# Kernel tuning notes

Hardware: AMD Instinct MI355X
Metric: run time of the kernel (lower is better)

## Reference

```python
import math
import jax, jax.numpy as jnp
import numpy as np

B, T, D = 2, 2048, 2048
H = 16
HD = D // H  # 128


def setup_inputs() -> dict:
    key = jax.random.key(0)
    k1, k2, k3 = jax.random.split(key, 3)
    x = jax.random.normal(k1, (B, T, D), dtype=jnp.float32)
    # Linear weights stored as [in, out] for x @ W (torch Linear weight is [out,in])
    w_attn = jax.random.normal(k2, (D, 3 * D), dtype=jnp.float32) * (1.0 / math.sqrt(D))
    w_proj = jax.random.normal(k3, (D, D), dtype=jnp.float32) * (1.0 / math.sqrt(D))
    return {"x": x, "w_attn": w_attn, "w_proj": w_proj}


def reference(x, w_attn, w_proj):
    Bc, Tc, Dc = x.shape
    qkv = x @ w_attn  # [B, T, 3D]
    q, k, v = jnp.split(qkv, 3, axis=2)
    # [B, H, T, HD]
    q = q.reshape(Bc, Tc, H, HD).transpose(0, 2, 1, 3)
    k = k.reshape(Bc, Tc, H, HD).transpose(0, 2, 1, 3)
    v = v.reshape(Bc, Tc, H, HD).transpose(0, 2, 1, 3)
    att = jnp.einsum('bhqd,bhkd->bhqk', q, k) * (1.0 / math.sqrt(HD))
    causal = jnp.tril(jnp.ones((Tc, Tc), dtype=bool))
    att = jnp.where(causal[None, None], att, -jnp.inf)
    att = jax.nn.softmax(att, axis=-1)
    y = jnp.einsum('bhqk,bhkd->bhqd', att, v)
    y = y.transpose(0, 2, 1, 3).reshape(Bc, Tc, Dc)
    return y @ w_proj
```

## Files before the change

kernel.cpp:

```cpp
#include <hip/hip_runtime.h>
#include <hip/hip_bf16.h>

#define B_ 2
#define T_ 2048
#define D_ 2048
#define H_ 16
#define HD_ 128
#define N3_ (3 * D_)
#define M_ (B_ * T_)

typedef __attribute__((ext_vector_type(8))) short short8;
typedef __attribute__((ext_vector_type(4))) short short4v;
typedef __attribute__((ext_vector_type(4))) float floatx4;

__device__ __forceinline__ ushort f2bf(float f) {
  unsigned int x = __float_as_uint(f);
  unsigned int r = (x + 0x7fffu + ((x >> 16) & 1u)) >> 16;
  return (ushort)r;
}

__device__ __forceinline__ void gload_lds16(const ushort* g, ushort* l) {
  __builtin_amdgcn_global_load_lds(
      (const __attribute__((address_space(1))) void*)g,
      (__attribute__((address_space(3))) void*)l, 16, 0, 0);
}

#define CONVB 4096
#define WATB 12288
#define WPTB 4096
__global__ __launch_bounds__(256) void prep(const float* __restrict__ x,
                                            const float* __restrict__ wa,
                                            const float* __restrict__ wp,
                                            ushort* __restrict__ xb,
                                            ushort* __restrict__ wt_attn,
                                            ushort* __restrict__ wt_proj) {
  __shared__ ushort tile[32][33];
  int bid = blockIdx.x;
  if (bid < CONVB) {
    int i = bid * 2048 + threadIdx.x * 8;
    union { ushort u[8]; short8 v; } t;
#pragma unroll
    for (int j = 0; j < 8; j++) t.u[j] = f2bf(x[i + j]);
    *(short8*)(xb + i) = t.v;
    return;
  }
  const float* in;
  ushort* out;
  int N, bx, by;
  if (bid < CONVB + WATB) {
    int id = bid - CONVB;
    N = N3_; bx = id % 192; by = id / 192; in = wa; out = wt_attn;
  } else {
    int id = bid - (CONVB + WATB);
    N = D_; bx = id & 63; by = id >> 6; in = wp; out = wt_proj;
  }
  int n0 = bx * 32, k0 = by * 32;
  int tx = threadIdx.x & 31, ty = threadIdx.x >> 5;
#pragma unroll
  for (int i = ty; i < 32; i += 8)
    tile[i][tx] = f2bf(in[(size_t)(k0 + i) * N + n0 + tx]);
  __syncthreads();
#pragma unroll
  for (int i = ty; i < 32; i += 8)
    out[(size_t)(n0 + i) * 2048 + k0 + tx] = tile[tx][i];
}

#define GBM 256
#define GBN 128
#define GBK 64
#define GKD 2048
#define GNT (GKD / GBK)
#define A_US (GBM * GBK)
#define B_US (GBN * GBK)
#define BUF_US (A_US + B_US)

struct GPtr {
  const ushort* a0;
  const ushort* b0;
};

__device__ __forceinline__ void gstage(const GPtr& gp, size_t kpos,
                                       ushort* slot, int w512) {
#pragma unroll
  for (int j = 0; j < 4; j++)
    gload_lds16(gp.a0 + kpos + (size_t)j * 64 * GKD, slot + j * 4096 + w512);
#pragma unroll
  for (int j = 0; j < 2; j++)
    gload_lds16(gp.b0 + kpos + (size_t)j * 64 * GKD,
                slot + A_US + j * 4096 + w512);
}

template <int VM, bool STG, bool BAR>
__device__ __forceinline__ void kstep(const GPtr& gp, size_t kpos,
                                      const ushort* Ac, const ushort* Bc,
                                      ushort* sslot, int w512,
                                      const int (&aoff)[4][2],
                                      const int (&boff)[4][2],
                                      floatx4 (&acc)[4][4]) {
  short8 af[4][2], bf[4][2];
#pragma unroll
  for (int kk = 0; kk < 2; kk++)
#pragma unroll
    for (int i = 0; i < 4; i++) {
      af[i][kk] = *(const short8*)(Ac + aoff[i][kk]);
      bf[i][kk] = *(const short8*)(Bc + boff[i][kk]);
    }
  if constexpr (STG) gstage(gp, kpos, sslot, w512);
  __builtin_amdgcn_s_setprio(1);
#pragma unroll
  for (int kk = 0; kk < 2; kk++)
#pragma unroll
    for (int mi = 0; mi < 4; mi++)
#pragma unroll
      for (int nj = 0; nj < 4; nj++)
        acc[mi][nj] = __builtin_amdgcn_mfma_f32_16x16x32_bf16(
            af[mi][kk], bf[nj][kk], acc[mi][nj], 0, 0, 0);
  __builtin_amdgcn_s_setprio(0);
  if constexpr (VM == 6) {
    asm volatile("s_waitcnt vmcnt(6)" ::: "memory");
  } else if constexpr (VM == 0) {
    asm volatile("s_waitcnt vmcnt(0)" ::: "memory");
  }
  if constexpr (BAR) {
    __builtin_amdgcn_sched_barrier(0);
    __builtin_amdgcn_s_barrier();
    __builtin_amdgcn_sched_barrier(0);
  }
}

__device__ __forceinline__ void gemm_core(const ushort* __restrict__ Ag,
                                          const ushort* __restrict__ Bg,
                                          ushort* lds, floatx4 (&acc)[4][4]) {
  int tid = threadIdx.x;
  int lane = tid & 63, wave = tid >> 6;
  int l16 = lane & 15, quad = lane >> 4;
  int wr = wave >> 1, wc = wave & 1;
  int w512 = wave * 512;

  int swz = ((tid & 7) ^ ((tid >> 3) & 7)) * 8;
  GPtr gp;
  gp.a0 = Ag + (size_t)(tid >> 3) * GKD + swz;
  gp.b0 = Bg + (size_t)(tid >> 3) * GKD + swz;

  int aoff[4][2], boff[4][2];
#pragma unroll
  for (int i = 0; i < 4; i++)
#pragma unroll
    for (int kk = 0; kk < 2; kk++) {
      int chk = ((kk * 4 + quad) ^ (l16 & 7)) * 8;
      aoff[i][kk] = (wr * 64 + i * 16 + l16) * GBK + chk;
      boff[i][kk] = (wc * 64 + i * 16 + l16) * GBK + chk;
    }

  gstage(gp, 0, lds, w512);
  gstage(gp, GBK, lds + BUF_US, w512);
  asm volatile("s_waitcnt vmcnt(6)" ::: "memory");
  __builtin_amdgcn_sched_barrier(0);
  __builtin_amdgcn_s_barrier();
  __builtin_amdgcn_sched_barrier(0);

  const ushort* cp = lds;
  ushort* sp = lds + 2 * BUF_US;
#pragma unroll 1
  for (int t = 0; t < GNT - 2; ++t) {
    kstep<6, true, true>(gp, (size_t)(t + 2) * GBK, cp, cp + A_US, sp, w512,
                         aoff, boff, acc);
    cp = (cp == lds + 2 * BUF_US) ? lds : cp + BUF_US;
    sp = (sp == lds + 2 * BUF_US) ? lds : sp + BUF_US;
  }
  kstep<0, false, true>(gp, 0, cp, cp + A_US, lds, w512, aoff, boff, acc);
  cp = (cp == lds + 2 * BUF_US) ? lds : cp + BUF_US;
  kstep<-1, false, false>(gp, 0, cp, cp + A_US, lds, w512, aoff, boff, acc);
}

__global__ __launch_bounds__(512, 2) void gemm_qkv(const ushort* __restrict__ X,
                                                   const ushort* __restrict__ Wt,
                                                   ushort* __restrict__ qb,
                                                   ushort* __restrict__ kb,
                                                   ushort* __restrict__ vst) {
  __shared__ __align__(16) ushort lds[3 * BUF_US];
  floatx4 acc[4][4];
#pragma unroll
  for (int i = 0; i < 4; i++)
#pragma unroll
    for (int j = 0; j < 4; j++) acc[i][j] = (floatx4){0.f, 0.f, 0.f, 0.f};

  int m0 = blockIdx.y * GBM, n0 = blockIdx.x * GBN;
  gemm_core(X + (size_t)m0 * GKD, Wt + (size_t)n0 * GKD, lds, acc);

  int tid = threadIdx.x, lane = tid & 63, wave = tid >> 6;
  int l16 = lane & 15, quad = lane >> 4, wr = wave >> 1, wc = wave & 1;
  int region = n0 >> 11;
  int h = (n0 & 2047) >> 7;
  int b = m0 >> 11, tb = m0 & 2047;
  if (region == 0) {
    ushort* P = qb + ((size_t)(b * H_ + h) * T_ + tb) * HD_;
#pragma unroll
    for (int mi = 0; mi < 4; mi++)
#pragma unroll
      for (int nj = 0; nj < 4; nj++)
#pragma unroll
        for (int r = 0; r < 4; r++)
          P[(size_t)(wr * 64 + mi * 16 + quad * 4 + r) * HD_ + wc * 64 +
            nj * 16 + l16] = f2bf(acc[mi][nj][r]);
  } else if (region == 1) {
    ushort* base = kb + (size_t)(b * H_ + h) * T_ * HD_;
#pragma unroll
    for (int mi = 0; mi < 4; mi++)
#pragma unroll
      for (int nj = 0; nj < 4; nj++) {
        int d = wc * 64 + nj * 16 + l16;
        int dhi = d >> 5, dlo = d & 31;
#pragma unroll
        for (int r = 0; r < 4; r++) {
          int t = tb + wr * 64 + mi * 16 + quad * 4 + r;
          int sK = ((quad * 4 + r) >> 1) & 3;
          base[(size_t)(t >> 6) * 8192 + dhi * 2048 + (t & 63) * 32 +
               (dlo ^ (sK << 3))] = f2bf(acc[mi][nj][r]);
        }
      }
  } else {
    ushort* base = vst + (size_t)(b * H_ + h) * T_ * HD_;
    int sd = ((l16 >> 1) & 3) << 3;
#pragma unroll
    for (int mi = 0; mi < 4; mi++)
#pragma unroll
      for (int r = 0; r < 4; r++) {
        int t = tb + wr * 64 + mi * 16 + quad * 4 + r;
        int c = t & 63;
        int p = (c & 15) * 4 + (c >> 4);
        size_t rowbase =
            (size_t)(t >> 6) * 8192 + (p >> 5) * 4096 + ((p & 31) ^ sd);
#pragma unroll
        for (int nj = 0; nj < 4; nj++) {
          int d = wc * 64 + nj * 16 + l16;
          base[rowbase + d * 32] = f2bf(acc[mi][nj][r]);
        }
      }
  }
}

__global__ __launch_bounds__(512, 2) void gemm_proj(const ushort* __restrict__ Y,
                                                    const ushort* __restrict__ Wt,
                                                    float* __restrict__ out) {
  __shared__ __align__(16) ushort lds[3 * BUF_US];
  floatx4 acc[4][4];
#pragma unroll
  for (int i = 0; i < 4; i++)
#pragma unroll
    for (int j = 0; j < 4; j++) acc[i][j] = (floatx4){0.f, 0.f, 0.f, 0.f};

  int m0 = blockIdx.y * GBM, n0 = blockIdx.x * GBN;
  gemm_core(Y + (size_t)m0 * GKD, Wt + (size_t)n0 * GKD, lds, acc);

  int tid = threadIdx.x, lane = tid & 63, wave = tid >> 6;
  int l16 = lane & 15, quad = lane >> 4, wr = wave >> 1, wc = wave & 1;
#pragma unroll
  for (int mi = 0; mi < 4; mi++)
#pragma unroll
    for (int nj = 0; nj < 4; nj++)
#pragma unroll
      for (int r = 0; r < 4; r++)
        out[(size_t)(m0 + wr * 64 + mi * 16 + quad * 4 + r) * D_ + n0 +
            wc * 64 + nj * 16 + l16] = acc[mi][nj][r];
}

__global__ __launch_bounds__(256) void attn128(const ushort* __restrict__ qb,
                                               const ushort* __restrict__ kst,
                                               const ushort* __restrict__ vst,
                                               ushort* __restrict__ y) {
  __shared__ ushort Ks[2][8192];
  __shared__ ushort Vs[2][8192];
  __shared__ ushort Ps[8192];
  int bid = blockIdx.x;
  int bh = bid & 31;
  int qt = (bid < 256) ? (bid >> 5) : (15 - ((bid - 256) >> 5));
  int q0 = qt * 128;
  int tid = threadIdx.x, lane = tid & 63, wave = tid >> 6;
  int l16 = lane & 15, quad = lane >> 4;
  int b = bh >> 4, h = bh & 15;
  const ushort* Q = qb + (size_t)bh * T_ * HD_;
  const ushort* Kt = kst + (size_t)bh * T_ * HD_;
  const ushort* Vt = vst + (size_t)bh * T_ * HD_;
  int qw0 = q0 + wave * 32;

  short8 qf[2][4];
#pragma unroll
  for (int mi = 0; mi < 2; mi++)
#pragma unroll
    for (int kk = 0; kk < 4; kk++)
      qf[mi][kk] = *(const short8*)(Q + (size_t)(qw0 + mi * 16 + l16) * HD_ +
                                    kk * 32 + quad * 8);

  floatx4 o[2][8];
#pragma unroll
  for (int mi = 0; mi < 2; mi++)
#pragma unroll
    for (int nt = 0; nt < 8; nt++) o[mi][nt] = (floatx4){0.f, 0.f, 0.f, 0.f};
  float lrow[2][4];
#pragma unroll
  for (int mi = 0; mi < 2; mi++)
#pragma unroll
    for (int r = 0; r < 4; r++) lrow[mi][r] = 0.f;

  const float scale2 = 0.08838834764831845f * 1.4426950408889634f;
  int ktiles = (q0 >> 6) + 2;
  int vchk = (quad ^ ((l16 >> 1) & 3)) * 8;

#pragma unroll
  for (int i = 0; i < 4; i++) {
    int g = i * 256 + wave * 64;
    gload_lds16(Kt + (g + lane) * 8, Ks[0] + g * 8);
    gload_lds16(Vt + (g + lane) * 8, Vs[0] + g * 8);
  }
  __syncthreads();

  int cur = 0;
  for (int tile = 0; tile < ktiles; tile++) {
    int kt = tile << 6;
    if (tile + 1 < ktiles) {
#pragma unroll
      for (int i = 0; i < 4; i++) {
        int g = i * 256 + wave * 64;
        gload_lds16(Kt + (size_t)(tile + 1) * 8192 + (g + lane) * 8,
                    Ks[cur ^ 1] + g * 8);
        gload_lds16(Vt + (size_t)(tile + 1) * 8192 + (g + lane) * 8,
                    Vs[cur ^ 1] + g * 8);
      }
    }
    if (kt <= qw0 + 31) {
      const ushort* Ksb = Ks[cur];
      const ushort* Vsb = Vs[cur];
      floatx4 s[2][4];
#pragma unroll
      for (int mi = 0; mi < 2; mi++)
#pragma unroll
        for (int ng = 0; ng < 4; ng++) s[mi][ng] = (floatx4){0.f, 0.f, 0.f, 0.f};
#pragma unroll
      for (int kk = 0; kk < 4; kk++) {
        short8 kf[4];
#pragma unroll
        for (int ng = 0; ng < 4; ng++)
          kf[ng] = *(const short8*)(Ksb + kk * 2048 + (ng * 16 + l16) * 32 +
                                    vchk);
        __builtin_amdgcn_s_setprio(1);
#pragma unroll
        for (int mi = 0; mi < 2; mi++)
#pragma unroll
          for (int ng = 0; ng < 4; ng++)
            s[mi][ng] = __builtin_amdgcn_mfma_f32_16x16x32_bf16(
                qf[mi][kk], kf[ng], s[mi][ng], 0, 0, 0);
        __builtin_amdgcn_s_setprio(0);
      }
      if (kt + 63 > qw0) {
#pragma unroll
        for (int mi = 0; mi < 2; mi++)
#pragma unroll
          for (int ng = 0; ng < 4; ng++)
#pragma unroll
            for (int r = 0; r < 4; r++) {
              int key = kt + ng * 16 + l16;
              int qr = qw0 + mi * 16 + quad * 4 + r;
              float p =
                  (key <= qr) ? exp2f(s[mi][ng][r] * scale2) : 0.f;
              s[mi][ng][r] = p;
              lrow[mi][r] += p;
            }
      } else {
#pragma unroll
        for (int mi = 0; mi < 2; mi++)
#pragma unroll
          for (int ng = 0; ng < 4; ng++)
#pragma unroll
            for (int r = 0; r < 4; r++) {
              float p = exp2f(s[mi][ng][r] * scale2);
              s[mi][ng][r] = p;
              lrow[mi][r] += p;
            }
      }
      ushort* Pw = Ps + wave * 2048;
#pragma unroll
      for (int mi = 0; mi < 2; mi++)
#pragma unroll
        for (int r = 0; r < 4; r++) {
          int row = mi * 16 + quad * 4 + r;
          short4v pk;
#pragma unroll
          for (int ng = 0; ng < 4; ng++) pk[ng] = (short)f2bf(s[mi][ng][r]);
          *(short4v*)(Pw + row * 64 + (((l16 >> 1) ^ (row & 7)) << 3) +
                      ((l16 & 1) << 2)) = pk;
        }
      short8 pf[2][2];
#pragma unroll
      for (int mi = 0; mi < 2; mi++)
#pragma unroll
        for (int kc = 0; kc < 2; kc++) {
          int row = mi * 16 + l16;
          pf[mi][kc] = *(const short8*)(
              Pw + row * 64 + ((((kc << 2) + quad) ^ (row & 7)) << 3));
        }
#pragma unroll
      for (int kc = 0; kc < 2; kc++) {
#pragma unroll
        for (int nt = 0; nt < 8; nt++) {
          short8 vf = *(const short8*)(Vsb + kc * 4096 + (nt * 16 + l16) * 32 +
                                       vchk);
          __builtin_amdgcn_s_setprio(1);
#pragma unroll
          for (int mi = 0; mi < 2; mi++)
            o[mi][nt] = __builtin_amdgcn_mfma_f32_16x16x32_bf16(
                pf[mi][kc], vf, o[mi][nt], 0, 0, 0);
          __builtin_amdgcn_s_setprio(0);
        }
      }
    }
    __syncthreads();
    cur ^= 1;
  }

#pragma unroll
  for (int off = 1; off < 16; off <<= 1)
#pragma unroll
    for (int mi = 0; mi < 2; mi++)
#pragma unroll
      for (int r = 0; r < 4; r++)
        lrow[mi][r] += __shfl_xor(lrow[mi][r], off);

#pragma unroll
  for (int mi = 0; mi < 2; mi++)
#pragma unroll
    for (int r = 0; r < 4; r++) {
      float inv = 1.f / lrow[mi][r];
      int t = qw0 + mi * 16 + quad * 4 + r;
#pragma unroll
      for (int nt = 0; nt < 8; nt++)
        y[((size_t)(b * T_ + t)) * D_ + h * HD_ + nt * 16 + l16] =
            f2bf(o[mi][nt][r] * inv);
    }
}

extern "C" void kernel_launch(void* const* d_in, const int* in_sizes, int n_in,
                              void* d_out, int out_size, void* d_ws,
                              size_t ws_size, hipStream_t stream) {
  const float* x = (const float*)d_in[0];
  const float* w_attn = (const float*)d_in[1];
  const float* w_proj = (const float*)d_in[2];
  float* out = (float*)d_out;

  char* ws = (char*)d_ws;
  ushort* wt_attn = (ushort*)(ws);
  ushort* wt_proj = (ushort*)(ws + 25165824);
  ushort* qb = (ushort*)(ws + 33554432);
  ushort* kb = (ushort*)(ws + 50331648);
  ushort* vst = (ushort*)(ws + 67108864);
  ushort* xb = (ushort*)(ws + 83886080);
  ushort* yb = xb;
  (void)in_sizes; (void)n_in; (void)out_size; (void)ws_size;

  prep<<<CONVB + WATB + WPTB, 256, 0, stream>>>(x, w_attn, w_proj, xb,
                                                wt_attn, wt_proj);
  gemm_qkv<<<dim3(N3_ / GBN, M_ / GBM), 512, 0, stream>>>(xb, wt_attn, qb, kb,
                                                          vst);
  attn128<<<B_ * H_ * (T_ / 128), 256, 0, stream>>>(qb, kb, vst, yb);
  gemm_proj<<<dim3(D_ / GBN, M_ / GBM), 512, 0, stream>>>(yb, wt_proj, out);
}
```

Before: 371.1 us.

## Read K/V tiles directly from global memory in attention, dropping LDS staging

The attention kernel no longer stages K and V tiles into double-buffered shared memory with a block-wide barrier per tile. Each wave now reads its K and V fragments straight from global memory and loops only over the key tiles its own rows need, so per-tile __syncthreads disappears and LDS use shrinks. The cost is that the four waves of a block each issue redundant global/L2 reads for the same K/V data, and there is no prefetch to hide that load latency. The GEMM macros are renamed with no functional change.

```diff
diff --git a/kernel.cpp b/kernel.cpp
--- a/kernel.cpp
+++ b/kernel.cpp
@@ -8,6 +8,7 @@
 #define HD_ 128
 #define N3_ (3 * D_)
 #define M_ (B_ * T_)
+#define GKD 2048
 
 typedef __attribute__((ext_vector_type(8))) short short8;
 typedef __attribute__((ext_vector_type(4))) short short4v;
@@ -65,21 +66,17 @@
     out[(size_t)(n0 + i) * 2048 + k0 + tx] = tile[tx][i];
 }
 
-#define GBM 256
-#define GBN 128
-#define GBK 64
-#define GKD 2048
-#define GNT (GKD / GBK)
-#define A_US (GBM * GBK)
-#define B_US (GBN * GBK)
-#define BUF_US (A_US + B_US)
-
-struct GPtr {
-  const ushort* a0;
-  const ushort* b0;
-};
-
-__device__ __forceinline__ void gstage(const GPtr& gp, size_t kpos,
+#define PBM 256
+#define PBN 128
+#define PBK 64
+#define PNT (GKD / PBK)
+#define PA_US (PBM * PBK)
+#define PB_US (PBN * PBK)
+#define PBUF (PA_US + PB_US)
+
+struct PPtr { const ushort *a0, *b0; };
+
+__device__ __forceinline__ void pstage(const PPtr& gp, size_t kpos,
                                        ushort* slot, int w512) {
 #pragma unroll
   for (int j = 0; j < 4; j++)
@@ -87,11 +84,11 @@
 #pragma unroll
   for (int j = 0; j < 2; j++)
     gload_lds16(gp.b0 + kpos + (size_t)j * 64 * GKD,
-                slot + A_US + j * 4096 + w512);
+                slot + PA_US + j * 4096 + w512);
 }
 
 template <int VM, bool STG, bool BAR>
-__device__ __forceinline__ void kstep(const GPtr& gp, size_t kpos,
+__device__ __forceinline__ void pstep(const PPtr& gp, size_t kpos,
                                       const ushort* Ac, const ushort* Bc,
                                       ushort* sslot, int w512,
                                       const int (&aoff)[4][2],
@@ -105,7 +102,7 @@
       af[i][kk] = *(const short8*)(Ac + aoff[i][kk]);
       bf[i][kk] = *(const short8*)(Bc + boff[i][kk]);
     }
-  if constexpr (STG) gstage(gp, kpos, sslot, w512);
+  if constexpr (STG) pstage(gp, kpos, sslot, w512);
   __builtin_amdgcn_s_setprio(1);
 #pragma unroll
   for (int kk = 0; kk < 2; kk++)
@@ -128,9 +125,9 @@
   }
 }
 
-__device__ __forceinline__ void gemm_core(const ushort* __restrict__ Ag,
-                                          const ushort* __restrict__ Bg,
-                                          ushort* lds, floatx4 (&acc)[4][4]) {
+__device__ __forceinline__ void pgemm_core(const ushort* __restrict__ Ag,
+                                           const ushort* __restrict__ Bg,
+                                           ushort* lds, floatx4 (&acc)[4][4]) {
   int tid = threadIdx.x;
   int lane = tid & 63, wave = tid >> 6;
   int l16 = lane & 15, quad = lane >> 4;
@@ -138,7 +135,7 @@
   int w512 = wave * 512;
 
   int swz = ((tid & 7) ^ ((tid >> 3) & 7)) * 8;
-  GPtr gp;
+  PPtr gp;
   gp.a0 = Ag + (size_t)(tid >> 3) * GKD + swz;
   gp.b0 = Bg + (size_t)(tid >> 3) * GKD + swz;
 
@@ -148,29 +145,29 @@
 #pragma unroll
     for (int kk = 0; kk < 2; kk++) {
       int chk = ((kk * 4 + quad) ^ (l16 & 7)) * 8;
-      aoff[i][kk] = (wr * 64 + i * 16 + l16) * GBK + chk;
-      boff[i][kk] = (wc * 64 + i * 16 + l16) * GBK + chk;
-    }
-
-  gstage(gp, 0, lds, w512);
-  gstage(gp, GBK, lds + BUF_US, w512);
+      aoff[i][kk] = (wr * 64 + i * 16 + l16) * PBK + chk;
+      boff[i][kk] = (wc * 64 + i * 16 + l16) * PBK + chk;
+    }
+
+  pstage(gp, 0, lds, w512);
+  pstage(gp, PBK, lds + PBUF, w512);
   asm volatile("s_waitcnt vmcnt(6)" ::: "memory");
   __builtin_amdgcn_sched_barrier(0);
   __builtin_amdgcn_s_barrier();
   __builtin_amdgcn_sched_barrier(0);
 
   const ushort* cp = lds;
-  ushort* sp = lds + 2 * BUF_US;
+  ushort* sp = lds + 2 * PBUF;
 #pragma unroll 1
-  for (int t = 0; t < GNT - 2; ++t) {
-    kstep<6, true, true>(gp, (size_t)(t + 2) * GBK, cp, cp + A_US, sp, w512,
+  for (int t = 0; t < PNT - 2; ++t) {
+    pstep<6, true, true>(gp, (size_t)(t + 2) * PBK, cp, cp + PA_US, sp, w512,
                          aoff, boff, acc);
-    cp = (cp == lds + 2 * BUF_US) ? lds : cp + BUF_US;
-    sp = (sp == lds + 2 * BUF_US) ? lds : sp + BUF_US;
-  }
-  kstep<0, false, true>(gp, 0, cp, cp + A_US, lds, w512, aoff, boff, acc);
-  cp = (cp == lds + 2 * BUF_US) ? lds : cp + BUF_US;
-  kstep<-1, false, false>(gp, 0, cp, cp + A_US, lds, w512, aoff, boff, acc);
+    cp = (cp == lds + 2 * PBUF) ? lds : cp + PBUF;
+    sp = (sp == lds + 2 * PBUF) ? lds : sp + PBUF;
+  }
+  pstep<0, false, true>(gp, 0, cp, cp + PA_US, lds, w512, aoff, boff, acc);
+  cp = (cp == lds + 2 * PBUF) ? lds : cp + PBUF;
+  pstep<-1, false, false>(gp, 0, cp, cp + PA_US, lds, w512, aoff, boff, acc);
 }
 
 __global__ __launch_bounds__(512, 2) void gemm_qkv(const ushort* __restrict__ X,
@@ -178,15 +175,15 @@
                                                    ushort* __restrict__ qb,
                                                    ushort* __restrict__ kb,
                                                    ushort* __restrict__ vst) {
-  __shared__ __align__(16) ushort lds[3 * BUF_US];
+  __shared__ __align__(16) ushort lds[3 * PBUF];
   floatx4 acc[4][4];
 #pragma unroll
   for (int i = 0; i < 4; i++)
 #pragma unroll
     for (int j = 0; j < 4; j++) acc[i][j] = (floatx4){0.f, 0.f, 0.f, 0.f};
 
-  int m0 = blockIdx.y * GBM, n0 = blockIdx.x * GBN;
-  gemm_core(X + (size_t)m0 * GKD, Wt + (size_t)n0 * GKD, lds, acc);
+  int m0 = blockIdx.y * PBM, n0 = blockIdx.x * PBN;
+  pgemm_core(X + (size_t)m0 * GKD, Wt + (size_t)n0 * GKD, lds, acc);
 
   int tid = threadIdx.x, lane = tid & 63, wave = tid >> 6;
   int l16 = lane & 15, quad = lane >> 4, wr = wave >> 1, wc = wave & 1;
@@ -243,15 +240,15 @@
 __global__ __launch_bounds__(512, 2) void gemm_proj(const ushort* __restrict__ Y,
                                                     const ushort* __restrict__ Wt,
                                                     float* __restrict__ out) {
-  __shared__ __align__(16) ushort lds[3 * BUF_US];
+  __shared__ __align__(16) ushort lds[3 * PBUF];
   floatx4 acc[4][4];
 #pragma unroll
   for (int i = 0; i < 4; i++)
 #pragma unroll
     for (int j = 0; j < 4; j++) acc[i][j] = (floatx4){0.f, 0.f, 0.f, 0.f};
 
-  int m0 = blockIdx.y * GBM, n0 = blockIdx.x * GBN;
-  gemm_core(Y + (size_t)m0 * GKD, Wt + (size_t)n0 * GKD, lds, acc);
+  int m0 = blockIdx.y * PBM, n0 = blockIdx.x * PBN;
+  pgemm_core(Y + (size_t)m0 * GKD, Wt + (size_t)n0 * GKD, lds, acc);
 
   int tid = threadIdx.x, lane = tid & 63, wave = tid >> 6;
   int l16 = lane & 15, quad = lane >> 4, wr = wave >> 1, wc = wave & 1;
@@ -269,8 +266,6 @@
                                                const ushort* __restrict__ kst,
                                                const ushort* __restrict__ vst,
                                                ushort* __restrict__ y) {
-  __shared__ ushort Ks[2][8192];
-  __shared__ ushort Vs[2][8192];
   __shared__ ushort Ps[8192];
   int bid = blockIdx.x;
   int bh = bid & 31;
@@ -304,118 +299,94 @@
     for (int r = 0; r < 4; r++) lrow[mi][r] = 0.f;
 
   const float scale2 = 0.08838834764831845f * 1.4426950408889634f;
-  int ktiles = (q0 >> 6) + 2;
   int vchk = (quad ^ ((l16 >> 1) & 3)) * 8;
-
-#pragma unroll
-  for (int i = 0; i < 4; i++) {
-    int g = i * 256 + wave * 64;
-    gload_lds16(Kt + (g + lane) * 8, Ks[0] + g * 8);
-    gload_lds16(Vt + (g + lane) * 8, Vs[0] + g * 8);
-  }
-  __syncthreads();
-
-  int cur = 0;
-  for (int tile = 0; tile < ktiles; tile++) {
+  ushort* Pw = Ps + wave * 2048;
+
+  int wtiles = qw0 >> 6;
+  for (int tile = 0; tile <= wtiles; tile++) {
     int kt = tile << 6;
-    if (tile + 1 < ktiles) {
-#pragma unroll
-      for (int i = 0; i < 4; i++) {
-        int g = i * 256 + wave * 64;
-        gload_lds16(Kt + (size_t)(tile + 1) * 8192 + (g + lane) * 8,
-                    Ks[cur ^ 1] + g * 8);
-        gload_lds16(Vt + (size_t)(tile + 1) * 8192 + (g + lane) * 8,
-                    Vs[cur ^ 1] + g * 8);
+    const ushort* Kg = Kt + (size_t)tile * 8192;
+    const ushort* Vg = Vt + (size_t)tile * 8192;
+    floatx4 s[2][4];
+#pragma unroll
+    for (int mi = 0; mi < 2; mi++)
+#pragma unroll
+      for (int ng = 0; ng < 4; ng++) s[mi][ng] = (floatx4){0.f, 0.f, 0.f, 0.f};
+#pragma unroll
+    for (int kk = 0; kk < 4; kk++) {
+      short8 kf[4];
+#pragma unroll
+      for (int ng = 0; ng < 4; ng++)
+        kf[ng] = *(const short8*)(Kg + kk * 2048 + (ng * 16 + l16) * 32 +
+                                  vchk);
+      __builtin_amdgcn_s_setprio(1);
+#pragma unroll
+      for (int mi = 0; mi < 2; mi++)
+#pragma unroll
+        for (int ng = 0; ng < 4; ng++)
+          s[mi][ng] = __builtin_amdgcn_mfma_f32_16x16x32_bf16(
+              qf[mi][kk], kf[ng], s[mi][ng], 0, 0, 0);
+      __builtin_amdgcn_s_setprio(0);
+    }
+    if (kt + 63 > qw0) {
+#pragma unroll
+      for (int mi = 0; mi < 2; mi++)
+#pragma unroll
+        for (int ng = 0; ng < 4; ng++)
+#pragma unroll
+          for (int r = 0; r < 4; r++) {
+            int key = kt + ng * 16 + l16;
+            int qr = qw0 + mi * 16 + quad * 4 + r;
+            float p = (key <= qr) ? exp2f(s[mi][ng][r] * scale2) : 0.f;
+            s[mi][ng][r] = p;
+            lrow[mi][r] += p;
+          }
+    } else {
+#pragma unroll
+      for (int mi = 0; mi < 2; mi++)
+#pragma unroll
+        for (int ng = 0; ng < 4; ng++)
+#pragma unroll
+          for (int r = 0; r < 4; r++) {
+            float p = exp2f(s[mi][ng][r] * scale2);
+            s[mi][ng][r] = p;
+            lrow[mi][r] += p;
+          }
+    }
+#pragma unroll
+    for (int mi = 0; mi < 2; mi++)
+#pragma unroll
+      for (int r = 0; r < 4; r++) {
+        int row = mi * 16 + quad * 4 + r;
+        short4v pk;
+#pragma unroll
+        for (int ng = 0; ng < 4; ng++) pk[ng] = (short)f2bf(s[mi][ng][r]);
+        *(short4v*)(Pw + row * 64 + (((l16 >> 1) ^ (row & 7)) << 3) +
+                    ((l16 & 1) << 2)) = pk;
       }
-    }
-    if (kt <= qw0 + 31) {
-      const ushort* Ksb = Ks[cur];
-      const ushort* Vsb = Vs[cur];
-      floatx4 s[2][4];
-#pragma unroll
-      for (int mi = 0; mi < 2; mi++)
-#pragma unroll
-        for (int ng = 0; ng < 4; ng++) s[mi][ng] = (floatx4){0.f, 0.f, 0.f, 0.f};
-#pragma unroll
-      for (int kk = 0; kk < 4; kk++) {
-        short8 kf[4];
-#pragma unroll
-        for (int ng = 0; ng < 4; ng++)
-          kf[ng] = *(const short8*)(Ksb + kk * 2048 + (ng * 16 + l16) * 32 +
-                                    vchk);
+    short8 pf[2][2];
+#pragma unroll
+    for (int mi = 0; mi < 2; mi++)
+#pragma unroll
+      for (int kc = 0; kc < 2; kc++) {
+        int row = mi * 16 + l16;
+        pf[mi][kc] = *(const short8*)(
+            Pw + row * 64 + ((((kc << 2) + quad) ^ (row & 7)) << 3));
+      }
+#pragma unroll
+    for (int kc = 0; kc < 2; kc++) {
+#pragma unroll
+      for (int nt = 0; nt < 8; nt++) {
+        short8 vf = *(const short8*)(Vg + kc * 4096 + (nt * 16 + l16) * 32 +
+                                     vchk);
         __builtin_amdgcn_s_setprio(1);
 #pragma unroll
         for (int mi = 0; mi < 2; mi++)
-#pragma unroll
-          for (int ng = 0; ng < 4; ng++)
-            s[mi][ng] = __builtin_amdgcn_mfma_f32_16x16x32_bf16(
-                qf[mi][kk], kf[ng], s[mi][ng], 0, 0, 0);
+          o[mi][nt] = __builtin_amdgcn_mfma_f32_16x16x32_bf16(
+              pf[mi][kc], vf, o[mi][nt], 0, 0, 0);
         __builtin_amdgcn_s_setprio(0);
       }
-      if (kt + 63 > qw0) {
-#pragma unroll
-        for (int mi = 0; mi < 2; mi++)
-#pragma unroll
-          for (int ng = 0; ng < 4; ng++)
-#pragma unroll
-            for (int r = 0; r < 4; r++) {
-              int key = kt + ng * 16 + l16;
-              int qr = qw0 + mi * 16 + quad * 4 + r;
-              float p =
-                  (key <= qr) ? exp2f(s[mi][ng][r] * scale2) : 0.f;
-              s[mi][ng][r] = p;
-              lrow[mi][r] += p;
-            }
-      } else {
-#pragma unroll
-        for (int mi = 0; mi < 2; mi++)
-#pragma unroll
-          for (int ng = 0; ng < 4; ng++)
-#pragma unroll
-            for (int r = 0; r < 4; r++) {
-              float p = exp2f(s[mi][ng][r] * scale2);
-              s[mi][ng][r] = p;
-              lrow[mi][r] += p;
-            }
-      }
-      ushort* Pw = Ps + wave * 2048;
-#pragma unroll
-      for (int mi = 0; mi < 2; mi++)
-#pragma unroll
-        for (int r = 0; r < 4; r++) {
-          int row = mi * 16 + quad * 4 + r;
-          short4v pk;
-#pragma unroll
-          for (int ng = 0; ng < 4; ng++) pk[ng] = (short)f2bf(s[mi][ng][r]);
-          *(short4v*)(Pw + row * 64 + (((l16 >> 1) ^ (row & 7)) << 3) +
-                      ((l16 & 1) << 2)) = pk;
-        }
-      short8 pf[2][2];
-#pragma unroll
-      for (int mi = 0; mi < 2; mi++)
-#pragma unroll
-        for (int kc = 0; kc < 2; kc++) {
-          int row = mi * 16 + l16;
-          pf[mi][kc] = *(const short8*)(
-              Pw + row * 64 + ((((kc << 2) + quad) ^ (row & 7)) << 3));
-        }
-#pragma unroll
-      for (int kc = 0; kc < 2; kc++) {
-#pragma unroll
-        for (int nt = 0; nt < 8; nt++) {
-          short8 vf = *(const short8*)(Vsb + kc * 4096 + (nt * 16 + l16) * 32 +
-                                       vchk);
-          __builtin_amdgcn_s_setprio(1);
-#pragma unroll
-          for (int mi = 0; mi < 2; mi++)
-            o[mi][nt] = __builtin_amdgcn_mfma_f32_16x16x32_bf16(
-                pf[mi][kc], vf, o[mi][nt], 0, 0, 0);
-          __builtin_amdgcn_s_setprio(0);
-        }
-      }
-    }
-    __syncthreads();
-    cur ^= 1;
+    }
   }
 
 #pragma unroll
@@ -459,8 +430,8 @@
 
   prep<<<CONVB + WATB + WPTB, 256, 0, stream>>>(x, w_attn, w_proj, xb,
                                                 wt_attn, wt_proj);
-  gemm_qkv<<<dim3(N3_ / GBN, M_ / GBM), 512, 0, stream>>>(xb, wt_attn, qb, kb,
+  gemm_qkv<<<dim3(N3_ / PBN, M_ / PBM), 512, 0, stream>>>(xb, wt_attn, qb, kb,
                                                           vst);
   attn128<<<B_ * H_ * (T_ / 128), 256, 0, stream>>>(qb, kb, vst, yb);
-  gemm_proj<<<dim3(D_ / GBN, M_ / GBM), 512, 0, stream>>>(yb, wt_proj, out);
-}
+  gemm_proj<<<dim3(D_ / PBN, M_ / PBM), 512, 0, stream>>>(yb, wt_proj, out);
+}
```

Measured after the change: 470.9 us. 26.9% more time.
